# Kernel optimization log

Measured on AMD Instinct MI355X. Metric: run time of the kernel, lower is better.

The kernel has to match this reference:

```python
import jax, jax.numpy as jnp
import numpy as np

B, S, D = 1, 1500, 1280
H = 20
HD = D // H
FFN = 5120
EPS = 1e-5


def _layer_norm(x, w, b):
    # manual LN as in the NPU graph: mean/var/div, eps=1e-5
    mean = jnp.mean(x, axis=-1, keepdims=True)
    var = jnp.mean((x - mean) ** 2, axis=-1, keepdims=True)
    return w * ((x - mean) / jnp.sqrt(var + EPS)) + b


def setup_inputs() -> dict:
    key = jax.random.key(0)
    ks = jax.random.split(key, 16)
    r = lambda k, shp, s=1.0: jax.random.normal(k, shp, dtype=jnp.float32) * s
    return {
        "x": r(ks[0], (B, S, D)),
        "ln1_w": jax.random.uniform(ks[1], (D,), dtype=jnp.float32),
        "ln1_b": r(ks[2], (D,), 0.02),
        "ln2_w": jax.random.uniform(ks[3], (D,), dtype=jnp.float32),
        "ln2_b": r(ks[4], (D,), 0.02),
        "wq": r(ks[5], (D, D), 0.02),
        "q_bias": r(ks[6], (D,), 0.02),
        "wk": r(ks[7], (D, D), 0.02),
        "wv": r(ks[8], (D, D), 0.02),
        "v_bias": r(ks[9], (D,), 0.02),
        "wo": r(ks[10], (D, D), 0.02),
        "out_bias": r(ks[11], (D,), 0.02),
        "w_fc1": r(ks[12], (FFN, D), 0.02),
        "fc1_bias": r(ks[13], (FFN,), 0.02),
        "w_fc2": r(ks[14], (D, FFN), 0.02),
        "fc2_bias": r(ks[15], (D,), 0.02),
    }


def reference(x, ln1_w, ln1_b, ln2_w, ln2_b, wq, q_bias, wk, wv, v_bias,
              wo, out_bias, w_fc1, fc1_bias, w_fc2, fc2_bias):
    scaling = HD ** -0.5
    residual = x
    h = _layer_norm(x.reshape(B * S, D), ln1_w, ln1_b)

    # self-attention (k_proj has no bias, as in Whisper)
    q = (h @ wq.T + q_bias) * scaling            # [S, D]
    k = h @ wk.T
    v = h @ wv.T + v_bias
    q = q.reshape(S, H, HD).transpose(1, 0, 2)   # [H, S, HD]
    k = k.reshape(S, H, HD).transpose(1, 0, 2)
    v = v.reshape(S, H, HD).transpose(1, 0, 2)

    attn = jnp.einsum('hqd,hkd->hqk', q, k)      # [H, S, S]
    attn = jax.nn.softmax(attn, axis=-1)
    ctx = jnp.einsum('hqk,hkd->hqd', attn, v)    # [H, S, HD]
    ctx = ctx.transpose(1, 0, 2).reshape(S, D)
    attn_out = ctx @ wo.T + out_bias

    h = residual + attn_out.reshape(B, S, D)

    residual = h
    h2 = _layer_norm(h.reshape(B * S, D), ln2_w, ln2_b)
    h2 = jax.nn.gelu(h2 @ w_fc1.T + fc1_bias, approximate=False)
    h2 = h2 @ w_fc2.T + fc2_bias
    return residual + h2.reshape(B, S, D)
```

## Files before the change

### kernel.cpp

```cpp
#include <hip/hip_runtime.h>
#include <math.h>

typedef unsigned short u16;
typedef __attribute__((ext_vector_type(8))) short bf16x8;
typedef __attribute__((ext_vector_type(4))) float f32x4;

#define S_VALID 1500
#define S_PAD   1536
#define DMODEL  1280
#define NHEAD   20
#define HDIM    64
#define FFND    5120
#define ZKEYS   768
#define NSPLIT_TILES 12

__device__ __forceinline__ u16 f2bf(float f) {
  union { float f; unsigned u; } v; v.f = f;
  unsigned r = v.u + 0x7fffu + ((v.u >> 16) & 1u);
  return (u16)(r >> 16);
}
__device__ __forceinline__ float bf2f(u16 h) {
  union { unsigned u; float f; } v; v.u = ((unsigned)h) << 16; return v.f;
}

template <int N>
__device__ __forceinline__ void wait_vmcnt() {
  if constexpr (N == 8)      asm volatile("s_waitcnt vmcnt(8)"  ::: "memory");
  else if constexpr (N == 6) asm volatile("s_waitcnt vmcnt(6)"  ::: "memory");
  else if constexpr (N == 4) asm volatile("s_waitcnt vmcnt(4)"  ::: "memory");
  else if constexpr (N == 3) asm volatile("s_waitcnt vmcnt(3)"  ::: "memory");
  else if constexpr (N == 2) asm volatile("s_waitcnt vmcnt(2)"  ::: "memory");
  else                       asm volatile("s_waitcnt vmcnt(0)"  ::: "memory");
}

__global__ void k_cvt4(const float* __restrict__ s0, const float* __restrict__ s1,
                       const float* __restrict__ s2, const float* __restrict__ s3,
                       u16* __restrict__ d0, u16* __restrict__ d1,
                       u16* __restrict__ d2, u16* __restrict__ d3, int n) {
  const float* in = (blockIdx.y == 0) ? s0 : (blockIdx.y == 1) ? s1 : (blockIdx.y == 2) ? s2 : s3;
  u16* out = (blockIdx.y == 0) ? d0 : (blockIdx.y == 1) ? d1 : (blockIdx.y == 2) ? d2 : d3;
  int i = (blockIdx.x * 256 + threadIdx.x) * 4;
  if (i >= n) return;
  float4 f = *(const float4*)(in + i);
  union { u16 s[4]; uint2 v; } o;
  o.s[0] = f2bf(f.x); o.s[1] = f2bf(f.y); o.s[2] = f2bf(f.z); o.s[3] = f2bf(f.w);
  *(uint2*)(out + i) = o.v;
}
__global__ void k_cvt2(const float* __restrict__ s0, const float* __restrict__ s1,
                       u16* __restrict__ d0, u16* __restrict__ d1, int n) {
  const float* in = (blockIdx.y == 0) ? s0 : s1;
  u16* out = (blockIdx.y == 0) ? d0 : d1;
  int i = (blockIdx.x * 256 + threadIdx.x) * 4;
  if (i >= n) return;
  float4 f = *(const float4*)(in + i);
  union { u16 s[4]; uint2 v; } o;
  o.s[0] = f2bf(f.x); o.s[1] = f2bf(f.y); o.s[2] = f2bf(f.z); o.s[3] = f2bf(f.w);
  *(uint2*)(out + i) = o.v;
}

__global__ __launch_bounds__(256) void k_ln(const float* __restrict__ x,
                                            const float* __restrict__ w,
                                            const float* __restrict__ b,
                                            u16* __restrict__ out, int rows_valid) {
  int r = blockIdx.x;
  int t = threadIdx.x;
  if (r >= rows_valid) {
    for (int i = t; i < DMODEL; i += 256) out[r * DMODEL + i] = 0;
    return;
  }
  const float* xr = x + (size_t)r * DMODEL;
  float vals[5]; float s = 0.f, ss = 0.f;
#pragma unroll
  for (int j = 0; j < 5; ++j) {
    float v = xr[t + j * 256]; vals[j] = v; s += v; ss += v * v;
  }
#pragma unroll
  for (int m = 1; m < 64; m <<= 1) { s += __shfl_xor(s, m); ss += __shfl_xor(ss, m); }
  __shared__ float ps[4], pss[4];
  int lane = t & 63, wv = t >> 6;
  if (lane == 0) { ps[wv] = s; pss[wv] = ss; }
  __syncthreads();
  s = ps[0] + ps[1] + ps[2] + ps[3];
  ss = pss[0] + pss[1] + pss[2] + pss[3];
  float mean = s * (1.f / DMODEL);
  float var = ss * (1.f / DMODEL) - mean * mean;
  float rstd = rsqrtf(var + 1e-5f);
#pragma unroll
  for (int j = 0; j < 5; ++j) {
    int i = t + j * 256;
    out[r * DMODEL + i] = f2bf(w[i] * ((vals[j] - mean) * rstd) + b[i]);
  }
}

struct EpiParams {
  const float* bias;
  const float* resid;
  float* outf;
  u16* outb;
  u16* q; u16* k; u16* vt;
  const float* qb; const float* vb;
  int mvalid;
};

template <int ROWS, int NT>
__device__ __forceinline__ void stage_tile(const u16* __restrict__ g, int ld,
                                           u16* lds, int t) {
  constexpr int ITERS = ROWS * 128 / (NT * 16);
#pragma unroll
  for (int i = 0; i < ITERS; ++i) {
    int off = i * (NT * 16) + t * 16;
    int row = off >> 7;
    int sp  = (off >> 4) & 7;
    int s   = sp ^ (row & 7);
    const u16* gp = g + row * ld + s * 8;
    u16* lp = lds + i * (NT * 8) + ((t >> 6) << 9);
    __builtin_amdgcn_global_load_lds((const __attribute__((address_space(1))) void*)gp,
                                     (__attribute__((address_space(3))) void*)lp,
                                     16, 0, 0);
  }
}

__device__ __forceinline__ bf16x8 ld_frag(const u16* lds, int row, int kk, int lane) {
  int slot = kk * 4 + (lane >> 4);
  int sp = slot ^ (row & 7);
  return *(const bf16x8*)(lds + row * 64 + sp * 8);
}

template <int BM, int BN, int EPI>
__global__ __launch_bounds__(512) void k_gemm(const u16* __restrict__ A,
                                              const u16* __restrict__ B,
                                              int N, int K, int lda, int ldb,
                                              EpiParams ep) {
  constexpr int FM = 2, FN = 2;
  constexpr int LOADS = (BM + BN) * 128 / (512 * 16);
  __shared__ __align__(128) u16 lds_a[2][BM * 64];
  __shared__ __align__(128) u16 lds_b[2][BN * 64];
  const int t = threadIdx.x, lane = t & 63, wid = t >> 6;
  const int wm = wid >> 2, wn = wid & 3;

  unsigned nwg = gridDim.x * gridDim.y;
  unsigned bid = blockIdx.y * gridDim.x + blockIdx.x;
  unsigned cpx = nwg >> 3;
  bid = (bid & 7u) * cpx + (bid >> 3);
  const int bm0 = (bid % gridDim.x) * BM, bn0 = (bid / gridDim.x) * BN;

  const int l15 = lane & 15, g4 = lane >> 4;

  f32x4 acc[FM][FN] = {};
  const size_t zk = (EPI == 4) ? (size_t)blockIdx.z * K : 0;
  const u16* Ab = A + (size_t)bm0 * lda + zk;
  const u16* Bb = B + (size_t)bn0 * ldb + zk;

  auto stage = [&](int kt, int buf) {
    stage_tile<BM, 512>(Ab + kt * 64, lda, &lds_a[buf][0], t);
    stage_tile<BN, 512>(Bb + kt * 64, ldb, &lds_b[buf][0], t);
  };

  const int NT = K >> 6;
  stage(0, 0);
  int buf = 0;

  for (int kt = 0; kt < NT; ++kt) {
    if (kt + 1 < NT) {
      stage(kt + 1, buf ^ 1);
      wait_vmcnt<LOADS>();
    } else {
      wait_vmcnt<0>();
    }
    __builtin_amdgcn_s_barrier();
    const u16* la = &lds_a[buf][0];
    const u16* lb = &lds_b[buf][0];
#pragma unroll
    for (int kk = 0; kk < 2; ++kk) {
      bf16x8 af[FM], bfr[FN];
#pragma unroll
      for (int i = 0; i < FM; ++i) af[i]  = ld_frag(la, wm * (BM / 2) + i * 16 + l15, kk, lane);
#pragma unroll
      for (int j = 0; j < FN; ++j) bfr[j] = ld_frag(lb, wn * (BN / 4) + j * 16 + l15, kk, lane);
#pragma unroll
      for (int i = 0; i < FM; ++i)
#pragma unroll
        for (int j = 0; j < FN; ++j)
          acc[i][j] = __builtin_amdgcn_mfma_f32_16x16x32_bf16(af[i], bfr[j], acc[i][j], 0, 0, 0);
    }
    __builtin_amdgcn_s_barrier();
    buf ^= 1;
  }

#pragma unroll
  for (int i = 0; i < FM; ++i)
#pragma unroll
    for (int j = 0; j < FN; ++j) {
      int n = bn0 + wn * (BN / 4) + j * 16 + l15;
      int mbase = bm0 + wm * (BM / 2) + i * 16 + g4 * 4;
      if constexpr (EPI == 0) {
        if (n >= 2 * DMODEL) {
          int nn = n - 2 * DMODEL;
          union { u16 s[4]; uint2 v2; } pk;
#pragma unroll
          for (int r = 0; r < 4; ++r) {
            int m = mbase + r;
            float val = (m < ep.mvalid) ? (acc[i][j][r] + ep.vb[nn]) : 0.f;
            pk.s[r] = f2bf(val);
          }
          *(uint2*)(ep.vt + (size_t)nn * S_PAD + mbase) = pk.v2;
        } else {
#pragma unroll
          for (int r = 0; r < 4; ++r) {
            int m = mbase + r;
            float v = acc[i][j][r];
            if (n < DMODEL) {
              float val = (m < ep.mvalid) ? (v + ep.qb[n]) * 0.125f : 0.f;
              ep.q[m * DMODEL + n] = f2bf(val);
            } else {
              int nn = n - DMODEL;
              ep.k[m * DMODEL + nn] = f2bf(m < ep.mvalid ? v : 0.f);
            }
          }
        }
      } else {
#pragma unroll
        for (int r = 0; r < 4; ++r) {
          int m = mbase + r;
          float v = acc[i][j][r];
          if constexpr (EPI == 2) {
            float xx = v + ep.bias[n];
            float gg = 0.5f * xx * (1.f + erff(xx * 0.70710678118f));
            ep.outb[(size_t)m * N + n] = f2bf(gg);
          } else if constexpr (EPI == 4) {
            ep.outf[((size_t)blockIdx.z * S_PAD + m) * DMODEL + n] = v;
          }
        }
      }
    }
}

__global__ __launch_bounds__(256) void k_red(const float* __restrict__ p,
                                             const float* __restrict__ bias,
                                             const float* __restrict__ resid,
                                             float* __restrict__ out) {
  int idx = blockIdx.x * 256 + threadIdx.x;
  if (idx >= S_VALID * (DMODEL / 4)) return;
  int m = idx / (DMODEL / 4), n4 = (idx % (DMODEL / 4)) * 4;
  float4 a  = *(const float4*)(p + (size_t)m * DMODEL + n4);
  float4 b  = *(const float4*)(p + ((size_t)S_PAD + m) * DMODEL + n4);
  float4 rs = *(const float4*)(resid + (size_t)m * DMODEL + n4);
  float4 bb = *(const float4*)(bias + n4);
  float4 o;
  o.x = a.x + b.x + rs.x + bb.x;
  o.y = a.y + b.y + rs.y + bb.y;
  o.z = a.z + b.z + rs.z + bb.z;
  o.w = a.w + b.w + rs.w + bb.w;
  *(float4*)(out + (size_t)m * DMODEL + n4) = o;
}

__global__ __launch_bounds__(256) void k_attn(const u16* __restrict__ q,
                                              const u16* __restrict__ k,
                                              const u16* __restrict__ vt,
                                              u16* __restrict__ o0,
                                              u16* __restrict__ o1,
                                              float2* __restrict__ ml) {
  __shared__ __align__(128) u16 kls[2][2][2048];
  __shared__ __align__(128) u16 vls[2][2][2048];
  const int t = threadIdx.x;
  const int lane = t & 63, wid = t >> 6;
  const int h = blockIdx.y, z = blockIdx.z;
  const int zb = z * ZKEYS;
  const int qbase = blockIdx.x * 64 + wid * 16;
  const int l15 = lane & 15, g = lane >> 4;

  const int srow = t >> 3;
  const int psl  = t & 7;
  const int slog = psl ^ (srow & 7);
  const int kperm = 8 * ((srow & 15) >> 2) + (srow & 3) + 4 * (srow >> 4);
  const int vd    = 2 * srow + (slog >> 2);
  const int vkoff = (slog & 3) * 8;
  const u16* kbasep = k + (size_t)kperm * DMODEL + h * HDIM + slog * 8;
  const u16* vbasep = vt + (size_t)(h * HDIM + vd) * S_PAD + vkoff;
  const int wbase = (t >> 6) << 9;

  bf16x8 qf[2];
#pragma unroll
  for (int half = 0; half < 2; ++half)
    qf[half] = *(const bf16x8*)(q + (qbase + l15) * DMODEL + h * HDIM + half * 32 + g * 8);

  auto stage = [&](int tt, int buf) {
#pragma unroll
    for (int u = 0; u < 2; ++u) {
      int keyoff = zb + tt * 64 + u * 32;
      __builtin_amdgcn_global_load_lds(
          (const __attribute__((address_space(1))) void*)(kbasep + (size_t)keyoff * DMODEL),
          (__attribute__((address_space(3))) void*)(&kls[buf][u][0] + wbase), 16, 0, 0);
      __builtin_amdgcn_global_load_lds(
          (const __attribute__((address_space(1))) void*)(vbasep + keyoff),
          (__attribute__((address_space(3))) void*)(&vls[buf][u][0] + wbase), 16, 0, 0);
    }
  };

  stage(0, 0);
  int buf = 0;

  float Mx = -1e30f, L = 0.f;
  f32x4 c[4] = {};

  for (int tt = 0; tt < NSPLIT_TILES; ++tt) {
    if (tt + 1 < NSPLIT_TILES) {
      stage(tt + 1, buf ^ 1);
      wait_vmcnt<4>();
    } else {
      wait_vmcnt<0>();
    }
    __builtin_amdgcn_s_barrier();

    f32x4 sc[2][2];
#pragma unroll
    for (int u = 0; u < 2; ++u)
#pragma unroll
      for (int s = 0; s < 2; ++s) {
        int row = 16 * s + l15;
        const u16* kb = &kls[buf][u][0];
        bf16x8 ka0 = *(const bf16x8*)(kb + row * 64 + ((g)     ^ (row & 7)) * 8);
        bf16x8 ka1 = *(const bf16x8*)(kb + row * 64 + ((4 + g) ^ (row & 7)) * 8);
        f32x4 zz = {};
        zz = __builtin_amdgcn_mfma_f32_16x16x32_bf16(ka0, qf[0], zz, 0, 0, 0);
        zz = __builtin_amdgcn_mfma_f32_16x16x32_bf16(ka1, qf[1], zz, 0, 0, 0);
        sc[u][s] = zz;
      }
    float pm = -1e30f;
#pragma unroll
    for (int u = 0; u < 2; ++u)
#pragma unroll
      for (int s = 0; s < 2; ++s)
#pragma unroll
        for (int r = 0; r < 4; ++r) {
          int kg = zb + tt * 64 + u * 32 + 8 * g + 4 * s + r;
          float v = (kg < S_VALID) ? sc[u][s][r] : -1e30f;
          sc[u][s][r] = v;
          pm = fmaxf(pm, v);
        }
    pm = fmaxf(pm, __shfl_xor(pm, 16));
    pm = fmaxf(pm, __shfl_xor(pm, 32));
    float Mn = fmaxf(Mx, pm);
    float fac = __expf(Mx - Mn);
    float p[2][8]; float rs = 0.f;
#pragma unroll
    for (int u = 0; u < 2; ++u)
#pragma unroll
      for (int s = 0; s < 2; ++s)
#pragma unroll
        for (int r = 0; r < 4; ++r) {
          float e = __expf(sc[u][s][r] - Mn);
          p[u][4 * s + r] = e; rs += e;
        }
    rs += __shfl_xor(rs, 16);
    rs += __shfl_xor(rs, 32);
    L = L * fac + rs; Mx = Mn;

    float facr[4];
#pragma unroll
    for (int r = 0; r < 4; ++r) facr[r] = __shfl(fac, g * 20 + r);
#pragma unroll
    for (int ch = 0; ch < 4; ++ch)
#pragma unroll
      for (int r = 0; r < 4; ++r) c[ch][r] *= facr[r];

    bf16x8 pa[2];
#pragma unroll
    for (int u = 0; u < 2; ++u)
#pragma unroll
      for (int j = 0; j < 8; ++j) pa[u][j] = (short)f2bf(p[u][j]);
#pragma unroll
    for (int ch = 0; ch < 4; ++ch) {
      int R = 8 * ch + (l15 >> 1);
      int sl = (l15 & 1) * 4 + g;
#pragma unroll
      for (int u = 0; u < 2; ++u) {
        bf16x8 vbf = *(const bf16x8*)(&vls[buf][u][0] + R * 64 + (sl ^ (R & 7)) * 8);
        c[ch] = __builtin_amdgcn_mfma_f32_16x16x32_bf16(pa[u], vbf, c[ch], 0, 0, 0);
      }
    }
    __builtin_amdgcn_s_barrier();
    buf ^= 1;
  }

  u16* op = z ? o1 : o0;
  if (g == 0) ml[(size_t)(z * NHEAD + h) * S_PAD + qbase + l15] = make_float2(Mx, L);
#pragma unroll
  for (int ch = 0; ch < 4; ++ch)
#pragma unroll
    for (int r = 0; r < 4; ++r) {
      int m = qbase + g * 4 + r;
      op[(size_t)m * DMODEL + h * HDIM + ch * 16 + l15] = f2bf(c[ch][r]);
    }
}

__global__ __launch_bounds__(256) void k_comb(u16* __restrict__ o0,
                                              const u16* __restrict__ o1,
                                              const float2* __restrict__ ml) {
  int idx = blockIdx.x * 256 + threadIdx.x;
  if (idx >= S_VALID * (DMODEL / 4)) return;
  int m = idx / (DMODEL / 4);
  int d = (idx % (DMODEL / 4)) * 4;
  int h = d >> 6;
  float2 a = ml[(size_t)h * S_PAD + m];
  float2 b = ml[(size_t)(NHEAD + h) * S_PAD + m];
  float M = fmaxf(a.x, b.x);
  float w0 = __expf(a.x - M), w1 = __expf(b.x - M);
  float inv = 1.f / (w0 * a.y + w1 * b.y);
  w0 *= inv; w1 *= inv;
  union { u16 s[4]; uint2 v; } A, B, O;
  A.v = *(const uint2*)(o0 + (size_t)m * DMODEL + d);
  B.v = *(const uint2*)(o1 + (size_t)m * DMODEL + d);
#pragma unroll
  for (int j = 0; j < 4; ++j)
    O.s[j] = f2bf(w0 * bf2f(A.s[j]) + w1 * bf2f(B.s[j]));
  *(uint2*)(o0 + (size_t)m * DMODEL + d) = O.v;
}

extern "C" void kernel_launch(void* const* d_in, const int* in_sizes, int n_in,
                              void* d_out, int out_size, void* d_ws, size_t ws_size,
                              hipStream_t stream) {
  const float* x    = (const float*)d_in[0];
  const float* ln1w = (const float*)d_in[1];
  const float* ln1b = (const float*)d_in[2];
  const float* ln2w = (const float*)d_in[3];
  const float* ln2b = (const float*)d_in[4];
  const float* wq   = (const float*)d_in[5];
  const float* qb   = (const float*)d_in[6];
  const float* wk   = (const float*)d_in[7];
  const float* wv   = (const float*)d_in[8];
  const float* vb   = (const float*)d_in[9];
  const float* wo   = (const float*)d_in[10];
  const float* ob   = (const float*)d_in[11];
  const float* wfc1 = (const float*)d_in[12];
  const float* fb1  = (const float*)d_in[13];
  const float* wfc2 = (const float*)d_in[14];
  const float* fb2  = (const float*)d_in[15];

  char* ws = (char*)d_ws;
  size_t off = 0;
  auto alloc = [&](size_t bytes) {
    void* p = ws + off; off += (bytes + 255) & ~(size_t)255; return p;
  };
  u16*   w_qkv = (u16*)alloc((size_t)3 * DMODEL * DMODEL * 2);
  u16*   w_o   = (u16*)alloc((size_t)DMODEL * DMODEL * 2);
  u16*   w_f1  = (u16*)alloc((size_t)FFND * DMODEL * 2);
  u16*   w_f2  = (u16*)alloc((size_t)DMODEL * FFND * 2);
  u16*   hbuf  = (u16*)alloc((size_t)S_PAD * DMODEL * 2);
  u16*   qbuf  = (u16*)alloc((size_t)S_PAD * DMODEL * 2);
  u16*   kbuf  = (u16*)alloc((size_t)S_PAD * DMODEL * 2);
  u16*   vtb   = (u16*)alloc((size_t)DMODEL * S_PAD * 2);
  u16*   ctxb  = (u16*)alloc((size_t)S_PAD * DMODEL * 2);
  float* res2  = (float*)alloc((size_t)S_PAD * DMODEL * 4);
  u16*   h2buf = (u16*)alloc((size_t)S_PAD * DMODEL * 2);
  u16*   gbuf  = (u16*)alloc((size_t)S_PAD * FFND * 2);
  float* skp   = (float*)hbuf;
  u16*    opart1 = (u16*)res2;
  float2* mlbuf  = (float2*)((char*)res2 + (size_t)S_PAD * DMODEL * 2);
  (void)ws_size; (void)n_in; (void)in_sizes; (void)out_size;

  const int nDD = DMODEL * DMODEL;
  const int nF  = FFND * DMODEL;
  k_cvt4<<<dim3(nDD / 1024, 4), 256, 0, stream>>>(
      wq, wk, wv, wo, w_qkv, w_qkv + (size_t)nDD, w_qkv + (size_t)2 * nDD, w_o, nDD);
  k_cvt2<<<dim3(nF / 1024, 2), 256, 0, stream>>>(wfc1, wfc2, w_f1, w_f2, nF);

  k_ln<<<S_PAD, 256, 0, stream>>>(x, ln1w, ln1b, hbuf, S_VALID);

  {
    EpiParams ep = {};
    ep.q = qbuf; ep.k = kbuf; ep.vt = vtb; ep.qb = qb; ep.vb = vb; ep.mvalid = S_VALID;
    k_gemm<64, 128, 0><<<dim3(S_PAD / 64, 3 * DMODEL / 128), 512, 0, stream>>>(
        hbuf, w_qkv, 3 * DMODEL, DMODEL, DMODEL, DMODEL, ep);
  }

  k_attn<<<dim3(S_PAD / 64, NHEAD, 2), 256, 0, stream>>>(
      qbuf, kbuf, vtb, ctxb, opart1, mlbuf);
  k_comb<<<(S_VALID * (DMODEL / 4) + 255) / 256, 256, 0, stream>>>(
      ctxb, opart1, mlbuf);

  {
    EpiParams ep = {};
    ep.outf = skp; ep.mvalid = S_VALID;
    k_gemm<64, 128, 4><<<dim3(S_PAD / 64, DMODEL / 128, 2), 512, 0, stream>>>(
        ctxb, w_o, DMODEL, DMODEL / 2, DMODEL, DMODEL, ep);
  }
  k_red<<<(S_VALID * (DMODEL / 4) + 255) / 256, 256, 0, stream>>>(
      skp, ob, x, res2);

  k_ln<<<S_PAD, 256, 0, stream>>>(res2, ln2w, ln2b, h2buf, S_VALID);

  {
    EpiParams ep = {};
    ep.bias = fb1; ep.outb = gbuf; ep.mvalid = S_VALID;
    k_gemm<64, 128, 2><<<dim3(S_PAD / 64, FFND / 128), 512, 0, stream>>>(
        h2buf, w_f1, FFND, DMODEL, DMODEL, DMODEL, ep);
  }

  {
    EpiParams ep = {};
    ep.outf = skp; ep.mvalid = S_VALID;
    k_gemm<64, 128, 4><<<dim3(S_PAD / 64, DMODEL / 128, 2), 512, 0, stream>>>(
        gbuf, w_f2, DMODEL, FFND / 2, FFND, FFND, ep);
  }
  k_red<<<(S_VALID * (DMODEL / 4) + 255) / 256, 256, 0, stream>>>(
      skp, fb2, res2, (float*)d_out);
}
```

Before: 188.3 us.

## Fuse fp32-to-bf16 weight conversion into GEMM B-tile staging

Removes the separate weight-conversion kernels. Each GEMM now loads fp32 weight tiles into registers, converts them to bf16 and writes them into LDS, with register prefetch overlapping the MFMA loop. The FFN GEMMs switch to a 256-thread 64x64 tile variant, and the split-K partial buffer gets its own allocation. This saves the extra weight read/write pass but doubles the global bytes per B tile. It also adds register pressure and an extra sync in the main loop, and weights tiles are re-converted by every M block.

```diff
diff --git a/kernel.cpp b/kernel.cpp
--- a/kernel.cpp
+++ b/kernel.cpp
@@ -27,35 +27,15 @@
 __device__ __forceinline__ void wait_vmcnt() {
   if constexpr (N == 8)      asm volatile("s_waitcnt vmcnt(8)"  ::: "memory");
   else if constexpr (N == 6) asm volatile("s_waitcnt vmcnt(6)"  ::: "memory");
+  else if constexpr (N == 5) asm volatile("s_waitcnt vmcnt(5)"  ::: "memory");
   else if constexpr (N == 4) asm volatile("s_waitcnt vmcnt(4)"  ::: "memory");
   else if constexpr (N == 3) asm volatile("s_waitcnt vmcnt(3)"  ::: "memory");
   else if constexpr (N == 2) asm volatile("s_waitcnt vmcnt(2)"  ::: "memory");
+  else if constexpr (N == 1) asm volatile("s_waitcnt vmcnt(1)"  ::: "memory");
   else                       asm volatile("s_waitcnt vmcnt(0)"  ::: "memory");
 }
-
-__global__ void k_cvt4(const float* __restrict__ s0, const float* __restrict__ s1,
-                       const float* __restrict__ s2, const float* __restrict__ s3,
-                       u16* __restrict__ d0, u16* __restrict__ d1,
-                       u16* __restrict__ d2, u16* __restrict__ d3, int n) {
-  const float* in = (blockIdx.y == 0) ? s0 : (blockIdx.y == 1) ? s1 : (blockIdx.y == 2) ? s2 : s3;
-  u16* out = (blockIdx.y == 0) ? d0 : (blockIdx.y == 1) ? d1 : (blockIdx.y == 2) ? d2 : d3;
-  int i = (blockIdx.x * 256 + threadIdx.x) * 4;
-  if (i >= n) return;
-  float4 f = *(const float4*)(in + i);
-  union { u16 s[4]; uint2 v; } o;
-  o.s[0] = f2bf(f.x); o.s[1] = f2bf(f.y); o.s[2] = f2bf(f.z); o.s[3] = f2bf(f.w);
-  *(uint2*)(out + i) = o.v;
-}
-__global__ void k_cvt2(const float* __restrict__ s0, const float* __restrict__ s1,
-                       u16* __restrict__ d0, u16* __restrict__ d1, int n) {
-  const float* in = (blockIdx.y == 0) ? s0 : s1;
-  u16* out = (blockIdx.y == 0) ? d0 : d1;
-  int i = (blockIdx.x * 256 + threadIdx.x) * 4;
-  if (i >= n) return;
-  float4 f = *(const float4*)(in + i);
-  union { u16 s[4]; uint2 v; } o;
-  o.s[0] = f2bf(f.x); o.s[1] = f2bf(f.y); o.s[2] = f2bf(f.z); o.s[3] = f2bf(f.w);
-  *(uint2*)(out + i) = o.v;
+__device__ __forceinline__ void wait_lgkm0() {
+  asm volatile("s_waitcnt lgkmcnt(0)" ::: "memory");
 }
 
 __global__ __launch_bounds__(256) void k_ln(const float* __restrict__ x,
@@ -94,17 +74,18 @@
 
 struct EpiParams {
   const float* bias;
-  const float* resid;
   float* outf;
   u16* outb;
   u16* q; u16* k; u16* vt;
   const float* qb; const float* vb;
+  const float* wq_; const float* wk_; const float* wv_;
+  const float* w0_;
   int mvalid;
 };
 
 template <int ROWS, int NT>
-__device__ __forceinline__ void stage_tile(const u16* __restrict__ g, int ld,
-                                           u16* lds, int t) {
+__device__ __forceinline__ void stage_tileA(const u16* __restrict__ g, int ld,
+                                            u16* lds, int t) {
   constexpr int ITERS = ROWS * 128 / (NT * 16);
 #pragma unroll
   for (int i = 0; i < ITERS; ++i) {
@@ -126,17 +107,18 @@
   return *(const bf16x8*)(lds + row * 64 + sp * 8);
 }
 
-template <int BM, int BN, int EPI>
-__global__ __launch_bounds__(512) void k_gemm(const u16* __restrict__ A,
-                                              const u16* __restrict__ B,
-                                              int N, int K, int lda, int ldb,
-                                              EpiParams ep) {
-  constexpr int FM = 2, FN = 2;
-  constexpr int LOADS = (BM + BN) * 128 / (512 * 16);
-  __shared__ __align__(128) u16 lds_a[2][BM * 64];
-  __shared__ __align__(128) u16 lds_b[2][BN * 64];
+template <int BM, int BN, int NTH, int WM, int WN, int EPI>
+__device__ __forceinline__ void gemm_body(const u16* __restrict__ A,
+                                          int N, int K, int lda, int ldb,
+                                          const EpiParams& ep,
+                                          u16* lds_a0, u16* lds_a1,
+                                          u16* lds_b0, u16* lds_b1) {
+  constexpr int FM = BM / (32 * WM) * 2, FN = BN / (32 * WN) * 2;
+  constexpr int AL = BM * 128 / (NTH * 16);
+  u16* lds_a[2] = { lds_a0, lds_a1 };
+  u16* lds_b[2] = { lds_b0, lds_b1 };
   const int t = threadIdx.x, lane = t & 63, wid = t >> 6;
-  const int wm = wid >> 2, wn = wid & 3;
+  const int wm = wid / WN, wn = wid % WN;
 
   unsigned nwg = gridDim.x * gridDim.y;
   unsigned bid = blockIdx.y * gridDim.x + blockIdx.x;
@@ -149,40 +131,82 @@
   f32x4 acc[FM][FN] = {};
   const size_t zk = (EPI == 4) ? (size_t)blockIdx.z * K : 0;
   const u16* Ab = A + (size_t)bm0 * lda + zk;
-  const u16* Bb = B + (size_t)bn0 * ldb + zk;
-
-  auto stage = [&](int kt, int buf) {
-    stage_tile<BM, 512>(Ab + kt * 64, lda, &lds_a[buf][0], t);
-    stage_tile<BN, 512>(Bb + kt * 64, ldb, &lds_b[buf][0], t);
+
+  const float* Bf;
+  if constexpr (EPI == 0) {
+    int sel = bn0 / DMODEL;
+    int rem = bn0 - sel * DMODEL;
+    Bf = (sel == 0 ? ep.wq_ : sel == 1 ? ep.wk_ : ep.wv_) + (size_t)rem * ldb;
+  } else {
+    Bf = ep.w0_ + (size_t)bn0 * ldb + zk;
+  }
+
+  int brow[2], bs[2];
+#pragma unroll
+  for (int i = 0; i < 2; ++i) {
+    int off = i * (NTH * 16) + t * 16;
+    int row = off >> 7, sp = (off >> 4) & 7;
+    brow[i] = row; bs[i] = sp ^ (row & 7);
+  }
+  float4 br[2][2];
+
+  auto issueB = [&](int kt) {
+#pragma unroll
+    for (int i = 0; i < 2; ++i) {
+      const float* gp = Bf + (size_t)brow[i] * ldb + kt * 64 + bs[i] * 8;
+      br[i][0] = *(const float4*)gp;
+      br[i][1] = *(const float4*)(gp + 4);
+    }
   };
+  auto writeB = [&](int buf) {
+#pragma unroll
+    for (int i = 0; i < 2; ++i) {
+      union { u16 s[8]; bf16x8 v; } pk;
+      const float* f0 = (const float*)&br[i][0];
+      const float* f1 = (const float*)&br[i][1];
+#pragma unroll
+      for (int j = 0; j < 4; ++j) { pk.s[j] = f2bf(f0[j]); pk.s[4 + j] = f2bf(f1[j]); }
+      *(bf16x8*)(lds_b[buf] + i * (NTH * 8) + t * 8) = pk.v;
+    }
+  };
 
   const int NT = K >> 6;
-  stage(0, 0);
+  issueB(0);
+  stage_tileA<BM, NTH>(Ab, lda, lds_a[0], t);
+  wait_vmcnt<AL>();
+  writeB(0);
   int buf = 0;
 
   for (int kt = 0; kt < NT; ++kt) {
     if (kt + 1 < NT) {
-      stage(kt + 1, buf ^ 1);
-      wait_vmcnt<LOADS>();
+      issueB(kt + 1);
+      stage_tileA<BM, NTH>(Ab + (kt + 1) * 64, lda, lds_a[buf ^ 1], t);
+      wait_vmcnt<4 + AL>();
     } else {
       wait_vmcnt<0>();
     }
+    wait_lgkm0();
     __builtin_amdgcn_s_barrier();
-    const u16* la = &lds_a[buf][0];
-    const u16* lb = &lds_b[buf][0];
+    const u16* la = lds_a[buf];
+    const u16* lb = lds_b[buf];
 #pragma unroll
     for (int kk = 0; kk < 2; ++kk) {
       bf16x8 af[FM], bfr[FN];
 #pragma unroll
-      for (int i = 0; i < FM; ++i) af[i]  = ld_frag(la, wm * (BM / 2) + i * 16 + l15, kk, lane);
-#pragma unroll
-      for (int j = 0; j < FN; ++j) bfr[j] = ld_frag(lb, wn * (BN / 4) + j * 16 + l15, kk, lane);
+      for (int i = 0; i < FM; ++i) af[i]  = ld_frag(la, wm * (BM / WM) + i * 16 + l15, kk, lane);
+#pragma unroll
+      for (int j = 0; j < FN; ++j) bfr[j] = ld_frag(lb, wn * (BN / WN) + j * 16 + l15, kk, lane);
 #pragma unroll
       for (int i = 0; i < FM; ++i)
 #pragma unroll
         for (int j = 0; j < FN; ++j)
           acc[i][j] = __builtin_amdgcn_mfma_f32_16x16x32_bf16(af[i], bfr[j], acc[i][j], 0, 0, 0);
     }
+    if (kt + 1 < NT) {
+      wait_vmcnt<AL>();
+      writeB(buf ^ 1);
+    }
+    wait_lgkm0();
     __builtin_amdgcn_s_barrier();
     buf ^= 1;
   }
@@ -191,8 +215,8 @@
   for (int i = 0; i < FM; ++i)
 #pragma unroll
     for (int j = 0; j < FN; ++j) {
-      int n = bn0 + wn * (BN / 4) + j * 16 + l15;
-      int mbase = bm0 + wm * (BM / 2) + i * 16 + g4 * 4;
+      int n = bn0 + wn * (BN / WN) + j * 16 + l15;
+      int mbase = bm0 + wm * (BM / WM) + i * 16 + g4 * 4;
       if constexpr (EPI == 0) {
         if (n >= 2 * DMODEL) {
           int nn = n - 2 * DMODEL;
@@ -233,6 +257,28 @@
         }
       }
     }
+}
+
+template <int BM, int BN, int EPI>
+__global__ __launch_bounds__(512) void k_gemm(const u16* __restrict__ A,
+                                              int N, int K, int lda, int ldb,
+                                              EpiParams ep) {
+  __shared__ __align__(128) u16 lds_a[2][BM * 64];
+  __shared__ __align__(128) u16 lds_b[2][BN * 64];
+  gemm_body<BM, BN, 512, 2, 4, EPI>(A, N, K, lda, ldb, ep,
+                                    &lds_a[0][0], &lds_a[1][0],
+                                    &lds_b[0][0], &lds_b[1][0]);
+}
+
+template <int BM, int BN, int EPI>
+__global__ __launch_bounds__(256) void k_gemm2(const u16* __restrict__ A,
+                                               int N, int K, int lda, int ldb,
+                                               EpiParams ep) {
+  __shared__ __align__(128) u16 lds_a[2][BM * 64];
+  __shared__ __align__(128) u16 lds_b[2][BN * 64];
+  gemm_body<BM, BN, 256, 2, 2, EPI>(A, N, K, lda, ldb, ep,
+                                    &lds_a[0][0], &lds_a[1][0],
+                                    &lds_b[0][0], &lds_b[1][0]);
 }
 
 __global__ __launch_bounds__(256) void k_red(const float* __restrict__ p,
@@ -442,10 +488,6 @@
   auto alloc = [&](size_t bytes) {
     void* p = ws + off; off += (bytes + 255) & ~(size_t)255; return p;
   };
-  u16*   w_qkv = (u16*)alloc((size_t)3 * DMODEL * DMODEL * 2);
-  u16*   w_o   = (u16*)alloc((size_t)DMODEL * DMODEL * 2);
-  u16*   w_f1  = (u16*)alloc((size_t)FFND * DMODEL * 2);
-  u16*   w_f2  = (u16*)alloc((size_t)DMODEL * FFND * 2);
   u16*   hbuf  = (u16*)alloc((size_t)S_PAD * DMODEL * 2);
   u16*   qbuf  = (u16*)alloc((size_t)S_PAD * DMODEL * 2);
   u16*   kbuf  = (u16*)alloc((size_t)S_PAD * DMODEL * 2);
@@ -454,24 +496,19 @@
   float* res2  = (float*)alloc((size_t)S_PAD * DMODEL * 4);
   u16*   h2buf = (u16*)alloc((size_t)S_PAD * DMODEL * 2);
   u16*   gbuf  = (u16*)alloc((size_t)S_PAD * FFND * 2);
-  float* skp   = (float*)hbuf;
+  float* skp   = (float*)alloc((size_t)2 * S_PAD * DMODEL * 4);
   u16*    opart1 = (u16*)res2;
   float2* mlbuf  = (float2*)((char*)res2 + (size_t)S_PAD * DMODEL * 2);
   (void)ws_size; (void)n_in; (void)in_sizes; (void)out_size;
 
-  const int nDD = DMODEL * DMODEL;
-  const int nF  = FFND * DMODEL;
-  k_cvt4<<<dim3(nDD / 1024, 4), 256, 0, stream>>>(
-      wq, wk, wv, wo, w_qkv, w_qkv + (size_t)nDD, w_qkv + (size_t)2 * nDD, w_o, nDD);
-  k_cvt2<<<dim3(nF / 1024, 2), 256, 0, stream>>>(wfc1, wfc2, w_f1, w_f2, nF);
-
   k_ln<<<S_PAD, 256, 0, stream>>>(x, ln1w, ln1b, hbuf, S_VALID);
 
   {
     EpiParams ep = {};
     ep.q = qbuf; ep.k = kbuf; ep.vt = vtb; ep.qb = qb; ep.vb = vb; ep.mvalid = S_VALID;
+    ep.wq_ = wq; ep.wk_ = wk; ep.wv_ = wv;
     k_gemm<64, 128, 0><<<dim3(S_PAD / 64, 3 * DMODEL / 128), 512, 0, stream>>>(
-        hbuf, w_qkv, 3 * DMODEL, DMODEL, DMODEL, DMODEL, ep);
+        hbuf, 3 * DMODEL, DMODEL, DMODEL, DMODEL, ep);
   }
 
   k_attn<<<dim3(S_PAD / 64, NHEAD, 2), 256, 0, stream>>>(
@@ -481,9 +518,9 @@
 
   {
     EpiParams ep = {};
-    ep.outf = skp; ep.mvalid = S_VALID;
+    ep.outf = skp; ep.mvalid = S_VALID; ep.w0_ = wo;
     k_gemm<64, 128, 4><<<dim3(S_PAD / 64, DMODEL / 128, 2), 512, 0, stream>>>(
-        ctxb, w_o, DMODEL, DMODEL / 2, DMODEL, DMODEL, ep);
+        ctxb, DMODEL, DMODEL / 2, DMODEL, DMODEL, ep);
   }
   k_red<<<(S_VALID * (DMODEL / 4) + 255) / 256, 256, 0, stream>>>(
       skp, ob, x, res2);
@@ -492,16 +529,16 @@
 
   {
     EpiParams ep = {};
-    ep.bias = fb1; ep.outb = gbuf; ep.mvalid = S_VALID;
-    k_gemm<64, 128, 2><<<dim3(S_PAD / 64, FFND / 128), 512, 0, stream>>>(
-        h2buf, w_f1, FFND, DMODEL, DMODEL, DMODEL, ep);
+    ep.bias = fb1; ep.outb = gbuf; ep.mvalid = S_VALID; ep.w0_ = wfc1;
+    k_gemm2<64, 64, 2><<<dim3(S_PAD / 64, FFND / 64), 256, 0, stream>>>(
+        h2buf, FFND, DMODEL, DMODEL, DMODEL, ep);
   }
 
   {
     EpiParams ep = {};
-    ep.outf = skp; ep.mvalid = S_VALID;
-    k_gemm<64, 128, 4><<<dim3(S_PAD / 64, DMODEL / 128, 2), 512, 0, stream>>>(
-        gbuf, w_f2, DMODEL, FFND / 2, FFND, FFND, ep);
+    ep.outf = skp; ep.mvalid = S_VALID; ep.w0_ = wfc2;
+    k_gemm2<64, 64, 4><<<dim3(S_PAD / 64, DMODEL / 64, 2), 256, 0, stream>>>(
+        gbuf, DMODEL, FFND / 2, FFND, FFND, ep);
   }
   k_red<<<(S_VALID * (DMODEL / 4) + 255) / 256, 256, 0, stream>>>(
       skp, fb2, res2, (float*)d_out);
```

Measured after the change: 312.0 us. 1.66x slower.
